# Kernel tuning notes

Hardware: AMD Instinct MI355X
Metric: run time of the kernel (lower is better)

The kernel has to match this reference:

```python
import jax, jax.numpy as jnp
import numpy as np

S, N, H = 2048, 32, 1024   # source len, batch, hidden_size
E = 1024                   # input_size (attention MLP width)


def setup_inputs() -> dict:
    key = jax.random.key(0)
    ks = jax.random.split(key, 8)
    sc_h = 1.0 / np.sqrt(H)
    sc_e = 1.0 / np.sqrt(E)
    return {
        "out_e": jax.random.normal(ks[0], (S, N, H), dtype=jnp.float32),
        "hidden_d": jax.random.normal(ks[1], (1, N, H), dtype=jnp.float32),
        "W1": jax.random.uniform(ks[2], (E, H), jnp.float32, -sc_h, sc_h),
        "b1": jax.random.uniform(ks[3], (E,), jnp.float32, -sc_h, sc_h),
        "W2": jax.random.uniform(ks[4], (E, H), jnp.float32, -sc_h, sc_h),
        "b2": jax.random.uniform(ks[5], (E,), jnp.float32, -sc_h, sc_h),
        "W3": jax.random.uniform(ks[6], (1, E), jnp.float32, -sc_e, sc_e),
        "b3": jax.random.uniform(ks[7], (1,), jnp.float32, -sc_e, sc_e),
    }


def reference(out_e, hidden_d, W1, b1, W2, b2, W3, b3):
    # hidden_d (1,N,H) broadcasts against out_e (S,N,H); no explicit repeat needed.
    h1 = jnp.einsum('one,he->onh'.replace('e', 'x'), hidden_d, W1.T) if False else None
    # linear1(hidden_d): (1,N,E); linear2(out_e): (S,N,E)
    proj = jnp.tanh(hidden_d @ W1.T + b1 + out_e @ W2.T + b2)      # (S,N,E)
    a = proj @ W3.T + b3                                           # (S,N,1)
    alpha = jax.nn.softmax(a, axis=0)                              # softmax over source dim S
    c = jnp.einsum('sne,snh->enh', alpha, out_e)                   # (1,N,H)
    return (c, alpha)
```

## Files before the change

### kernel.cpp

```cpp
#include <hip/hip_runtime.h>
#include <hip/hip_bf16.h>
#include <stdint.h>

constexpr int kS = 2048;
constexpr int kN = 32;
constexpr int kH = 1024;
constexpr int kE = 1024;
constexpr int kM = kS * kN;

constexpr int BM = 128;
constexpr int BE = 128;
constexpr int BK = 64;
constexpr int KSTEPS = kH / BK;

typedef __bf16 bf16x8 __attribute__((ext_vector_type(8)));
typedef float f32x4 __attribute__((ext_vector_type(4)));

__device__ __forceinline__ float tanh_fast(float x) {
    float e = __expf(2.0f * x);
    return 1.0f - 2.0f / (e + 1.0f);
}

__device__ __forceinline__ uint32_t f2bf_rne(float f) {
    uint32_t u = __builtin_bit_cast(uint32_t, f);
    u += 0x7FFFu + ((u >> 16) & 1u);
    return u >> 16;
}

__device__ __forceinline__ uint32_t pack2bf(float lo, float hi) {
    return f2bf_rne(lo) | (f2bf_rne(hi) << 16);
}

__device__ __forceinline__ void gl_lds16(const void* g, void* l) {
    __builtin_amdgcn_global_load_lds(
        (const __attribute__((address_space(1))) uint32_t*)g,
        (__attribute__((address_space(3))) uint32_t*)l, 16, 0, 0);
}

__global__ __launch_bounds__(256) void k0_cvtA(const float* __restrict__ in,
                                               unsigned short* __restrict__ out) {
    size_t i = (size_t)blockIdx.x * 256 + threadIdx.x;
    float4 v = ((const float4*)in)[i];
    uint2 o;
    o.x = pack2bf(v.x, v.y);
    o.y = pack2bf(v.z, v.w);
    ((uint2*)out)[i] = o;
}

__global__ __launch_bounds__(64) void k1_h1c(const float* __restrict__ hd,
                                             const float* __restrict__ W1,
                                             const float* __restrict__ b1,
                                             const float* __restrict__ b2,
                                             float* __restrict__ h1c) {
    int e = blockIdx.x;
    int lane = threadIdx.x;
    const float4* wrow = (const float4*)(W1 + (size_t)e * kH);
    float4 w[4];
#pragma unroll
    for (int q = 0; q < 4; ++q) w[q] = wrow[lane + q * 64];
    float bb = b1[e] + b2[e];
    for (int n = 0; n < kN; ++n) {
        const float4* hrow = (const float4*)(hd + (size_t)n * kH);
        float p = 0.f;
#pragma unroll
        for (int q = 0; q < 4; ++q) {
            float4 h4 = hrow[lane + q * 64];
            p += w[q].x * h4.x + w[q].y * h4.y + w[q].z * h4.z + w[q].w * h4.w;
        }
#pragma unroll
        for (int o = 32; o; o >>= 1) p += __shfl_xor(p, o);
        if (lane == 0) h1c[n * kE + e] = p + bb;
    }
}

__global__ __launch_bounds__(256) void k2_cvt(const float* __restrict__ W2,
                                              unsigned short* __restrict__ W2b) {
    int i = blockIdx.x * 256 + threadIdx.x;
    float4 v = ((const float4*)W2)[i];
    uint2 o;
    o.x = pack2bf(v.x, v.y);
    o.y = pack2bf(v.z, v.w);
    ((uint2*)W2b)[i] = o;
}

template <bool DIRECT>
__global__ __launch_bounds__(256, 2) void k3_gemm(const float* __restrict__ out_e,
                                                  const unsigned short* __restrict__ Abf,
                                                  const unsigned short* __restrict__ W2b,
                                                  const float* __restrict__ h1c,
                                                  const float* __restrict__ W3,
                                                  float* __restrict__ a_ws) {
    __shared__ __align__(16) unsigned short Abuf[2][BM * BK];
    __shared__ __align__(16) unsigned short Bbuf[2][BE * BK];

    const int tid = threadIdx.x;
    const int lane = tid & 63;
    const int w = tid >> 6;
    const int wr = w >> 1, wc = w & 1;
    const int l15 = lane & 15, lhi = lane >> 4;
    const int rowBase = (blockIdx.x >> 3) * BM;
    const int colBase = (blockIdx.x & 7) * BE;

    f32x4 acc[4][4];
#pragma unroll
    for (int m = 0; m < 4; ++m)
#pragma unroll
        for (int n = 0; n < 4; ++n)
#pragma unroll
            for (int j = 0; j < 4; ++j) {
                int rl = wr * 64 + m * 16 + lhi * 4 + j;
                int e = colBase + wc * 64 + n * 16 + l15;
                acc[m][n][j] = h1c[((rowBase + rl) & (kN - 1)) * kE + e];
            }

    const int r8 = lane >> 3;
    const int schunk = (lane & 7) ^ r8;
    auto stage_dma = [&](const unsigned short* src, int gRowBase, int ks, int buf,
                         unsigned short(*ldsArr)[BM * BK]) {
#pragma unroll
        for (int i = 0; i < 4; ++i) {
            int row = w * 32 + i * 8 + r8;
            const void* g = src + (size_t)(gRowBase + row) * kH + ks * BK + schunk * 8;
            void* l = (char*)ldsArr[buf] + w * 4096 + i * 1024;
            gl_lds16(g, l);
        }
    };

    auto stageA_load = [&](int ks, float4* regs) {
#pragma unroll
        for (int t = 0; t < 8; ++t) {
            int li = t * 256 + tid;
            int arow = li >> 4, akf = (li & 15) * 4;
            regs[t] = *(const float4*)(out_e + (size_t)(rowBase + arow) * kH + ks * BK + akf);
        }
    };
    auto stageB_load = [&](int ks, uint4* regs) {
#pragma unroll
        for (int t = 0; t < 4; ++t) {
            int li = t * 256 + tid;
            int brow = li >> 3, bk8 = (li & 7) * 8;
            regs[t] = *(const uint4*)(W2b + (size_t)(colBase + brow) * kH + ks * BK + bk8);
        }
    };
    auto stageA_write = [&](int buf, float4* regs) {
        char* base = (char*)Abuf[buf];
#pragma unroll
        for (int t = 0; t < 8; ++t) {
            int li = t * 256 + tid;
            int arow = li >> 4, akf = (li & 15) * 4;
            int off = arow * 128 + ((akf * 2) ^ ((arow & 7) << 4));
            uint2 val;
            val.x = pack2bf(regs[t].x, regs[t].y);
            val.y = pack2bf(regs[t].z, regs[t].w);
            *(uint2*)(base + off) = val;
        }
    };
    auto stageB_write = [&](int buf, uint4* regs) {
        char* base = (char*)Bbuf[buf];
#pragma unroll
        for (int t = 0; t < 4; ++t) {
            int li = t * 256 + tid;
            int brow = li >> 3, bk8 = (li & 7) * 8;
            int off = brow * 128 + ((bk8 * 2) ^ ((brow & 7) << 4));
            *(uint4*)(base + off) = regs[t];
        }
    };

    auto compute = [&](int cur) {
        const char* Ab = (const char*)Abuf[cur];
        const char* Bb = (const char*)Bbuf[cur];
        bf16x8 af[2][4], bfr[2][4];
#pragma unroll
        for (int kk = 0; kk < 2; ++kk) {
            int kb = (kk * 32 + lhi * 8) * 2;
#pragma unroll
            for (int m = 0; m < 4; ++m) {
                int row = wr * 64 + m * 16 + l15;
                uint4 v = *(const uint4*)(Ab + row * 128 + (kb ^ ((row & 7) << 4)));
                af[kk][m] = __builtin_bit_cast(bf16x8, v);
            }
#pragma unroll
            for (int n = 0; n < 4; ++n) {
                int row = wc * 64 + n * 16 + l15;
                uint4 v = *(const uint4*)(Bb + row * 128 + (kb ^ ((row & 7) << 4)));
                bfr[kk][n] = __builtin_bit_cast(bf16x8, v);
            }
        }
#pragma unroll
        for (int kk = 0; kk < 2; ++kk)
#pragma unroll
            for (int m = 0; m < 4; ++m)
#pragma unroll
                for (int n = 0; n < 4; ++n)
                    acc[m][n] = __builtin_amdgcn_mfma_f32_16x16x32_bf16(af[kk][m], bfr[kk][n],
                                                                        acc[m][n], 0, 0, 0);
    };

    if (DIRECT) {
        stage_dma(Abf, rowBase, 0, 0, Abuf);
        stage_dma(W2b, colBase, 0, 0, Bbuf);
        __syncthreads();
        int cur = 0;
#pragma unroll 4
        for (int ks = 0; ks < KSTEPS; ++ks) {
            if (ks + 1 < KSTEPS) {
                stage_dma(Abf, rowBase, ks + 1, cur ^ 1, Abuf);
                stage_dma(W2b, colBase, ks + 1, cur ^ 1, Bbuf);
            }
            compute(cur);
            __syncthreads();
            cur ^= 1;
        }
    } else {
        {
            float4 ar[8]; uint4 br[4];
            stageA_load(0, ar); stageB_load(0, br);
            stageA_write(0, ar); stageB_write(0, br);
        }
        __syncthreads();
        int cur = 0;
        for (int ks = 0; ks < KSTEPS; ++ks) {
            float4 ar[8]; uint4 br[4];
            if (ks + 1 < KSTEPS) { stageA_load(ks + 1, ar); stageB_load(ks + 1, br); }
            compute(cur);
            __syncthreads();
            if (ks + 1 < KSTEPS) {
                stageA_write(cur ^ 1, ar);
                stageB_write(cur ^ 1, br);
                __syncthreads();
                cur ^= 1;
            }
        }
    }

    float w3v[4];
#pragma unroll
    for (int n = 0; n < 4; ++n) w3v[n] = W3[colBase + wc * 64 + n * 16 + l15];
    float rs[4][4];
#pragma unroll
    for (int m = 0; m < 4; ++m)
#pragma unroll
        for (int j = 0; j < 4; ++j) {
            float v = 0.f;
#pragma unroll
            for (int n = 0; n < 4; ++n) v += w3v[n] * tanh_fast(acc[m][n][j]);
#pragma unroll
            for (int o = 1; o < 16; o <<= 1) v += __shfl_xor(v, o);
            rs[m][j] = v;
        }
    if (l15 == 0) {
#pragma unroll
        for (int m = 0; m < 4; ++m)
#pragma unroll
            for (int j = 0; j < 4; ++j)
                atomicAdd(&a_ws[rowBase + wr * 64 + m * 16 + lhi * 4 + j], rs[m][j]);
    }
}

__global__ __launch_bounds__(256) void k4_softmax(const float* __restrict__ a_ws,
                                                  float* __restrict__ alpha) {
    int n = blockIdx.x;
    int tid = threadIdx.x;
    __shared__ float red[4];
    float v[8];
    float mx = -1e30f;
#pragma unroll
    for (int i = 0; i < 8; ++i) {
        v[i] = a_ws[(i * 256 + tid) * kN + n];
        mx = fmaxf(mx, v[i]);
    }
#pragma unroll
    for (int o = 32; o; o >>= 1) mx = fmaxf(mx, __shfl_xor(mx, o));
    if ((tid & 63) == 0) red[tid >> 6] = mx;
    __syncthreads();
    mx = fmaxf(fmaxf(red[0], red[1]), fmaxf(red[2], red[3]));
    float sum = 0.f;
#pragma unroll
    for (int i = 0; i < 8; ++i) { v[i] = __expf(v[i] - mx); sum += v[i]; }
#pragma unroll
    for (int o = 32; o; o >>= 1) sum += __shfl_xor(sum, o);
    __syncthreads();
    if ((tid & 63) == 0) red[tid >> 6] = sum;
    __syncthreads();
    sum = red[0] + red[1] + red[2] + red[3];
    float inv = 1.0f / sum;
#pragma unroll
    for (int i = 0; i < 8; ++i) alpha[(i * 256 + tid) * kN + n] = v[i] * inv;
}

__global__ __launch_bounds__(256) void k5_part(const float* __restrict__ out_e,
                                               const float* __restrict__ alpha,
                                               float* __restrict__ c_part) {
    int n = blockIdx.x & 31;
    int sc = blockIdx.x >> 5;
    int tid = threadIdx.x;
    float4 acc = make_float4(0.f, 0.f, 0.f, 0.f);
    for (int s = sc * 128; s < sc * 128 + 128; ++s) {
        float al = alpha[s * kN + n];
        float4 x = *(const float4*)(out_e + ((size_t)s * kN + n) * kH + tid * 4);
        acc.x += al * x.x; acc.y += al * x.y; acc.z += al * x.z; acc.w += al * x.w;
    }
    *(float4*)(c_part + ((size_t)sc * kN + n) * kH + tid * 4) = acc;
}

__global__ __launch_bounds__(256) void k6_reduce(const float* __restrict__ c_part,
                                                 float* __restrict__ c) {
    int idx = blockIdx.x * 256 + threadIdx.x;
    float4 acc = make_float4(0.f, 0.f, 0.f, 0.f);
#pragma unroll
    for (int scn = 0; scn < 16; ++scn) {
        float4 x = ((const float4*)c_part)[scn * 8192 + idx];
        acc.x += x.x; acc.y += x.y; acc.z += x.z; acc.w += x.w;
    }
    ((float4*)c)[idx] = acc;
}

extern "C" void kernel_launch(void* const* d_in, const int* in_sizes, int n_in,
                              void* d_out, int out_size, void* d_ws, size_t ws_size,
                              hipStream_t stream) {
    const float* out_e = (const float*)d_in[0];
    const float* hidden_d = (const float*)d_in[1];
    const float* W1 = (const float*)d_in[2];
    const float* b1 = (const float*)d_in[3];
    const float* W2 = (const float*)d_in[4];
    const float* b2 = (const float*)d_in[5];
    const float* W3 = (const float*)d_in[6];

    float* out = (float*)d_out;
    float* c_out = out;
    float* alpha_out = out + kN * kH;

    char* ws = (char*)d_ws;
    unsigned short* W2b = (unsigned short*)ws;
    float* h1c = (float*)(ws + (2u << 20));
    float* a_ws = (float*)(ws + (2u << 20) + (128u << 10));
    float* c_part = (float*)(ws + (2u << 20) + (384u << 10));
    unsigned short* Abf = (unsigned short*)(ws + (5u << 20));
    const size_t needed = (5ull << 20) + (size_t)kM * kH * 2;
    const bool direct = ws_size >= needed;

    k1_h1c<<<kE, 64, 0, stream>>>(hidden_d, W1, b1, b2, h1c);
    k2_cvt<<<(kE * kH / 4) / 256, 256, 0, stream>>>(W2, W2b);
    if (direct) k0_cvtA<<<(int)((size_t)kM * kH / 4 / 256), 256, 0, stream>>>(out_e, Abf);
    (void)hipMemsetAsync(a_ws, 0, kM * sizeof(float), stream);
    if (direct)
        k3_gemm<true><<<(kM / BM) * (kE / BE), 256, 0, stream>>>(out_e, Abf, W2b, h1c, W3, a_ws);
    else
        k3_gemm<false><<<(kM / BM) * (kE / BE), 256, 0, stream>>>(out_e, Abf, W2b, h1c, W3, a_ws);
    k4_softmax<<<kN, 256, 0, stream>>>(a_ws, alpha_out);
    k5_part<<<16 * kN, 256, 0, stream>>>(out_e, alpha_out, c_part);
    k6_reduce<<<32, 256, 0, stream>>>(c_part, c_out);
}
```

Baseline: 683.3 us.

## Single-buffer GEMM LDS for higher occupancy, remap tiles, read bf16 copy in context pass

The GEMM drops from double-buffered to single-buffered LDS and raises launch bounds to 4 blocks per CU. The aim is to hide load latency through more resident blocks instead of software pipelining. Block-to-tile mapping is remapped so that consecutive blocks (bid>>3) walk row tiles within one column tile (bid&7). The context-vector pass now reads the bf16 copy of out_e instead of fp32, halving its traffic, and uses 32 source chunks instead of 16, with the reduce kernel and workspace offsets adjusted to match. The risks are that the serialized load/compute inside each block is not covered by the extra occupancy, and that the context output loses precision from using bf16 inputs.

```diff
diff --git a/kernel.cpp b/kernel.cpp
--- a/kernel.cpp
+++ b/kernel.cpp
@@ -12,6 +12,8 @@
 constexpr int BE = 128;
 constexpr int BK = 64;
 constexpr int KSTEPS = kH / BK;
+constexpr int NTILES = (kM / BM) * (kE / BE);
+constexpr int TPX = NTILES / 8;
 
 typedef __bf16 bf16x8 __attribute__((ext_vector_type(8)));
 typedef float f32x4 __attribute__((ext_vector_type(4)));
@@ -84,22 +86,24 @@
 }
 
 template <bool DIRECT>
-__global__ __launch_bounds__(256, 2) void k3_gemm(const float* __restrict__ out_e,
+__global__ __launch_bounds__(256, 4) void k3_gemm(const float* __restrict__ out_e,
                                                   const unsigned short* __restrict__ Abf,
                                                   const unsigned short* __restrict__ W2b,
                                                   const float* __restrict__ h1c,
                                                   const float* __restrict__ W3,
                                                   float* __restrict__ a_ws) {
-    __shared__ __align__(16) unsigned short Abuf[2][BM * BK];
-    __shared__ __align__(16) unsigned short Bbuf[2][BE * BK];
+    __shared__ __align__(16) unsigned short Abuf[BM * BK];
+    __shared__ __align__(16) unsigned short Bbuf[BE * BK];
 
     const int tid = threadIdx.x;
     const int lane = tid & 63;
     const int w = tid >> 6;
     const int wr = w >> 1, wc = w & 1;
     const int l15 = lane & 15, lhi = lane >> 4;
-    const int rowBase = (blockIdx.x >> 3) * BM;
-    const int colBase = (blockIdx.x & 7) * BE;
+    const int bid = blockIdx.x;
+    const int tile = (bid & 7) * TPX + (bid >> 3);
+    const int rowBase = (tile >> 3) * BM;
+    const int colBase = (tile & 7) * BE;
 
     f32x4 acc[4][4];
 #pragma unroll
@@ -115,13 +119,13 @@
 
     const int r8 = lane >> 3;
     const int schunk = (lane & 7) ^ r8;
-    auto stage_dma = [&](const unsigned short* src, int gRowBase, int ks, int buf,
-                         unsigned short(*ldsArr)[BM * BK]) {
+    auto stage_dma = [&](const unsigned short* src, int gRowBase, int ks,
+                         unsigned short* lds) {
 #pragma unroll
         for (int i = 0; i < 4; ++i) {
             int row = w * 32 + i * 8 + r8;
             const void* g = src + (size_t)(gRowBase + row) * kH + ks * BK + schunk * 8;
-            void* l = (char*)ldsArr[buf] + w * 4096 + i * 1024;
+            void* l = (char*)lds + w * 4096 + i * 1024;
             gl_lds16(g, l);
         }
     };
@@ -142,8 +146,8 @@
             regs[t] = *(const uint4*)(W2b + (size_t)(colBase + brow) * kH + ks * BK + bk8);
         }
     };
-    auto stageA_write = [&](int buf, float4* regs) {
-        char* base = (char*)Abuf[buf];
+    auto stageA_write = [&](float4* regs) {
+        char* base = (char*)Abuf;
 #pragma unroll
         for (int t = 0; t < 8; ++t) {
             int li = t * 256 + tid;
@@ -155,8 +159,8 @@
             *(uint2*)(base + off) = val;
         }
     };
-    auto stageB_write = [&](int buf, uint4* regs) {
-        char* base = (char*)Bbuf[buf];
+    auto stageB_write = [&](uint4* regs) {
+        char* base = (char*)Bbuf;
 #pragma unroll
         for (int t = 0; t < 4; ++t) {
             int li = t * 256 + tid;
@@ -166,9 +170,9 @@
         }
     };
 
-    auto compute = [&](int cur) {
-        const char* Ab = (const char*)Abuf[cur];
-        const char* Bb = (const char*)Bbuf[cur];
+    auto compute = [&]() {
+        const char* Ab = (const char*)Abuf;
+        const char* Bb = (const char*)Bbuf;
         bf16x8 af[2][4], bfr[2][4];
 #pragma unroll
         for (int kk = 0; kk < 2; ++kk) {
@@ -197,38 +201,33 @@
     };
 
     if (DIRECT) {
-        stage_dma(Abf, rowBase, 0, 0, Abuf);
-        stage_dma(W2b, colBase, 0, 0, Bbuf);
+        stage_dma(Abf, rowBase, 0, Abuf);
+        stage_dma(W2b, colBase, 0, Bbuf);
         __syncthreads();
-        int cur = 0;
-#pragma unroll 4
         for (int ks = 0; ks < KSTEPS; ++ks) {
+            compute();
+            __syncthreads();
             if (ks + 1 < KSTEPS) {
-                stage_dma(Abf, rowBase, ks + 1, cur ^ 1, Abuf);
-                stage_dma(W2b, colBase, ks + 1, cur ^ 1, Bbuf);
-            }
-            compute(cur);
-            __syncthreads();
-            cur ^= 1;
+                stage_dma(Abf, rowBase, ks + 1, Abuf);
+                stage_dma(W2b, colBase, ks + 1, Bbuf);
+                __syncthreads();
+            }
         }
     } else {
         {
             float4 ar[8]; uint4 br[4];
             stageA_load(0, ar); stageB_load(0, br);
-            stageA_write(0, ar); stageB_write(0, br);
+            stageA_write(ar); stageB_write(br);
         }
         __syncthreads();
-        int cur = 0;
         for (int ks = 0; ks < KSTEPS; ++ks) {
             float4 ar[8]; uint4 br[4];
             if (ks + 1 < KSTEPS) { stageA_load(ks + 1, ar); stageB_load(ks + 1, br); }
-            compute(cur);
+            compute();
             __syncthreads();
             if (ks + 1 < KSTEPS) {
-                stageA_write(cur ^ 1, ar);
-                stageB_write(cur ^ 1, br);
+                stageA_write(ar); stageB_write(br);
                 __syncthreads();
-                cur ^= 1;
             }
         }
     }
@@ -288,17 +287,27 @@
     for (int i = 0; i < 8; ++i) alpha[(i * 256 + tid) * kN + n] = v[i] * inv;
 }
 
+template <bool BF>
 __global__ __launch_bounds__(256) void k5_part(const float* __restrict__ out_e,
+                                               const unsigned short* __restrict__ Abf,
                                                const float* __restrict__ alpha,
                                                float* __restrict__ c_part) {
     int n = blockIdx.x & 31;
     int sc = blockIdx.x >> 5;
     int tid = threadIdx.x;
     float4 acc = make_float4(0.f, 0.f, 0.f, 0.f);
-    for (int s = sc * 128; s < sc * 128 + 128; ++s) {
+    for (int s = sc * 64; s < sc * 64 + 64; ++s) {
         float al = alpha[s * kN + n];
-        float4 x = *(const float4*)(out_e + ((size_t)s * kN + n) * kH + tid * 4);
-        acc.x += al * x.x; acc.y += al * x.y; acc.z += al * x.z; acc.w += al * x.w;
+        if (BF) {
+            uint2 v = *(const uint2*)(Abf + ((size_t)s * kN + n) * kH + tid * 4);
+            acc.x += al * __builtin_bit_cast(float, v.x << 16);
+            acc.y += al * __builtin_bit_cast(float, v.x & 0xFFFF0000u);
+            acc.z += al * __builtin_bit_cast(float, v.y << 16);
+            acc.w += al * __builtin_bit_cast(float, v.y & 0xFFFF0000u);
+        } else {
+            float4 x = *(const float4*)(out_e + ((size_t)s * kN + n) * kH + tid * 4);
+            acc.x += al * x.x; acc.y += al * x.y; acc.z += al * x.z; acc.w += al * x.w;
+        }
     }
     *(float4*)(c_part + ((size_t)sc * kN + n) * kH + tid * 4) = acc;
 }
@@ -308,7 +317,7 @@
     int idx = blockIdx.x * 256 + threadIdx.x;
     float4 acc = make_float4(0.f, 0.f, 0.f, 0.f);
 #pragma unroll
-    for (int scn = 0; scn < 16; ++scn) {
+    for (int scn = 0; scn < 32; ++scn) {
         float4 x = ((const float4*)c_part)[scn * 8192 + idx];
         acc.x += x.x; acc.y += x.y; acc.z += x.z; acc.w += x.w;
     }
@@ -331,12 +340,17 @@
     float* alpha_out = out + kN * kH;
 
     char* ws = (char*)d_ws;
-    unsigned short* W2b = (unsigned short*)ws;
-    float* h1c = (float*)(ws + (2u << 20));
-    float* a_ws = (float*)(ws + (2u << 20) + (128u << 10));
-    float* c_part = (float*)(ws + (2u << 20) + (384u << 10));
-    unsigned short* Abf = (unsigned short*)(ws + (5u << 20));
-    const size_t needed = (5ull << 20) + (size_t)kM * kH * 2;
+    const size_t oW2b = 0;
+    const size_t oH1c = 2ull << 20;
+    const size_t oAws = oH1c + (128ull << 10);
+    const size_t oCpt = oAws + (256ull << 10);
+    const size_t oAbf = oCpt + (4ull << 20);
+    unsigned short* W2b = (unsigned short*)(ws + oW2b);
+    float* h1c = (float*)(ws + oH1c);
+    float* a_ws = (float*)(ws + oAws);
+    float* c_part = (float*)(ws + oCpt);
+    unsigned short* Abf = (unsigned short*)(ws + oAbf);
+    const size_t needed = oAbf + (size_t)kM * kH * 2;
     const bool direct = ws_size >= needed;
 
     k1_h1c<<<kE, 64, 0, stream>>>(hidden_d, W1, b1, b2, h1c);
@@ -344,10 +358,13 @@
     if (direct) k0_cvtA<<<(int)((size_t)kM * kH / 4 / 256), 256, 0, stream>>>(out_e, Abf);
     (void)hipMemsetAsync(a_ws, 0, kM * sizeof(float), stream);
     if (direct)
-        k3_gemm<true><<<(kM / BM) * (kE / BE), 256, 0, stream>>>(out_e, Abf, W2b, h1c, W3, a_ws);
+        k3_gemm<true><<<NTILES, 256, 0, stream>>>(out_e, Abf, W2b, h1c, W3, a_ws);
     else
-        k3_gemm<false><<<(kM / BM) * (kE / BE), 256, 0, stream>>>(out_e, Abf, W2b, h1c, W3, a_ws);
+        k3_gemm<false><<<NTILES, 256, 0, stream>>>(out_e, Abf, W2b, h1c, W3, a_ws);
     k4_softmax<<<kN, 256, 0, stream>>>(a_ws, alpha_out);
-    k5_part<<<16 * kN, 256, 0, stream>>>(out_e, alpha_out, c_part);
+    if (direct)
+        k5_part<true><<<32 * kN, 256, 0, stream>>>(out_e, Abf, alpha_out, c_part);
+    else
+        k5_part<false><<<32 * kN, 256, 0, stream>>>(out_e, Abf, alpha_out, c_part);
     k6_reduce<<<32, 256, 0, stream>>>(c_part, c_out);
 }
```

New measurement: 605.1 us. -11.5%, faster.
